# Optimization experiments

Measured on AMD Instinct MI355X. Metric: run time of the kernel, lower is better.

The kernel has to match this reference:

```python
import jax, jax.numpy as jnp
import numpy as np
from jax import lax

B, S, E, H = 4, 1024, 512, 8
D = E // H


def setup_inputs() -> dict:
    key = jax.random.key(0)
    k1, k2, k3 = jax.random.split(key, 3)
    source = jax.random.normal(k1, (B, S, E), dtype=jnp.float32)
    target = jax.random.normal(k2, (B, S, E), dtype=jnp.float32)
    # orthogonal-initialized positional encoder [1, H, 1, D]; random rows are a fine stand-in
    enc = jax.random.normal(k3, (1, H, 1, D), dtype=jnp.float32)
    enc = enc / jnp.linalg.norm(enc, axis=-1, keepdims=True)
    return {
        "source": source,
        "target": target,
        "encoder": enc,
        "alpha": jnp.float32(1.0),
        "beta": jnp.float32(1.0),
        "gamma": jnp.float32(2.0),
    }


def _split_heads(x):
    b, s, e = x.shape
    return x.reshape(b, s, H, e // H).transpose(0, 2, 1, 3)  # [B,H,S,D]


def reference(source, target, encoder, alpha, beta, gamma):
    q = _split_heads(source)  # [B,H,S,D]
    k = _split_heads(target)  # [B,H,S,D]
    pe = encoder[0, :, 0, :]  # [H,D]

    # --- grammar (time) attention: sequential tanh recurrence over t ---
    def step(cc, k_t):
        # cc, k_t: [B,H,D]
        cc = jnp.tanh(cc * pe)
        out = jnp.einsum('bhsd,bhd->bhs', q, cc)  # [B,H,S]
        return k_t * cc, out  # decay_rate = 0.0

    cc0 = k[:, :, 0, :]                      # initial cumulative context
    k_ts = jnp.moveaxis(k, 2, 0)             # [S,B,H,D]
    _, outs = lax.scan(step, cc0, k_ts)      # outs: [S,B,H,S]
    grammar = jnp.moveaxis(outs, 0, 3) / jnp.sqrt(jnp.float32(D))  # [B,H,S,S]
    grammar = jax.nn.softmax(grammar, axis=-1)

    # --- semantic attention ---
    semantic = jnp.einsum('bhsd,bhtd->bhst', q, k) / 100.0  # [B,H,S,S]

    w = jax.nn.softmax((alpha * semantic + beta * grammar) / gamma, axis=-1)

    # merge_heads: [B,H,S,S] -> [B,S,H*S]
    wm = w.transpose(0, 2, 1, 3).reshape(B, S, H * S)
    # output: wm^T @ target -> [B, H*S, E]
    return jnp.matmul(wm.transpose(0, 2, 1), target)
```

## Files before the change

kernel.cpp:

```cpp
#include <hip/hip_runtime.h>
#include <hip/hip_bf16.h>
#include <stdint.h>

#define S_LEN 1024
#define E_DIM 512
#define H_NUM 8
#define D_DIM 64
#define B_NUM 4
#define BH_NUM 32

using s16x8 = __attribute__((ext_vector_type(8))) short;
using f32x4 = __attribute__((ext_vector_type(4))) float;
using us4   = __attribute__((ext_vector_type(4))) unsigned short;

typedef const __attribute__((address_space(1))) uint32_t gas_uint;
typedef __attribute__((address_space(3))) uint32_t las_uint;

static __device__ __forceinline__ unsigned short f2bf(float f) {
  __hip_bfloat16 h = __float2bfloat16(f);
  return __builtin_bit_cast(unsigned short, h);
}
static __device__ __forceinline__ float bf2f(unsigned short u) {
  return __bfloat162float(__builtin_bit_cast(__hip_bfloat16, u));
}

#define NB_RECUR 8
#define NB_PACK  2048
#define NB_TR    512

__global__ __launch_bounds__(256) void k_prep(const float* __restrict__ src,
                                              const float* __restrict__ tgt,
                                              const float* __restrict__ enc,
                                              __hip_bfloat16* __restrict__ qb,
                                              __hip_bfloat16* __restrict__ kb,
                                              __hip_bfloat16* __restrict__ cb,
                                              __hip_bfloat16* __restrict__ tT) {
  __shared__ float tile[64][65];
  const int bid = blockIdx.x;
  const int tid = threadIdx.x;

  if (bid < NB_RECUR) {
    int g = bid * 256 + tid;
    int d = g & 63;
    int bh = g >> 6;
    int h = bh & 7;
    int b = bh >> 3;
    float pe = enc[h * D_DIM + d];
    float pe2 = 2.0f * pe;
    const float* tp = tgt + (size_t)b * S_LEN * E_DIM + h * D_DIM + d;
    __hip_bfloat16* cp = cb + (size_t)bh * S_LEN * D_DIM + d;

    constexpr int CH = 32;
    float bufA[CH], bufB[CH];
#pragma unroll
    for (int i = 0; i < CH; ++i) bufA[i] = tp[(size_t)i * E_DIM];
    float cc = bufA[0];

#pragma unroll 1
    for (int ch = 0; ch < S_LEN / CH; ch += 2) {
      if (ch + 1 < S_LEN / CH) {
#pragma unroll
        for (int i = 0; i < CH; ++i)
          bufB[i] = tp[(size_t)((ch + 1) * CH + i) * E_DIM];
      }
#pragma unroll
      for (int i = 0; i < CH; ++i) {
        float m = cc * pe2;
        float e = __expf(-fabsf(m));
        float th = __builtin_copysignf((1.0f - e) * __builtin_amdgcn_rcpf(1.0f + e), m);
        cp[(size_t)(ch * CH + i) * D_DIM] = __float2bfloat16(th);
        cc = bufA[i] * th;
      }
      if (ch + 2 < S_LEN / CH) {
#pragma unroll
        for (int i = 0; i < CH; ++i)
          bufA[i] = tp[(size_t)((ch + 2) * CH + i) * E_DIM];
      }
#pragma unroll
      for (int i = 0; i < CH; ++i) {
        float m = cc * pe2;
        float e = __expf(-fabsf(m));
        float th = __builtin_copysignf((1.0f - e) * __builtin_amdgcn_rcpf(1.0f + e), m);
        cp[(size_t)((ch + 1) * CH + i) * D_DIM] = __float2bfloat16(th);
        cc = bufB[i] * th;
      }
    }
  } else if (bid < NB_RECUR + NB_PACK) {
    size_t i4 = ((size_t)(bid - NB_RECUR) * 256 + tid) * 4;
    float4 s4 = *reinterpret_cast<const float4*>(src + i4);
    float4 t4 = *reinterpret_cast<const float4*>(tgt + i4);
    int e = (int)(i4 & 511);
    size_t bs = i4 >> 9;
    int s = (int)(bs & 1023);
    int b = (int)(bs >> 10);
    int h = e >> 6, d = e & 63;
    size_t o = (((size_t)(b * H_NUM + h) * S_LEN) + s) * D_DIM + d;
    us4 qv = {f2bf(s4.x), f2bf(s4.y), f2bf(s4.z), f2bf(s4.w)};
    us4 kv = {f2bf(t4.x), f2bf(t4.y), f2bf(t4.z), f2bf(t4.w)};
    *reinterpret_cast<us4*>(qb + o) = qv;
    *reinterpret_cast<us4*>(kb + o) = kv;
  } else {
    int lb = bid - (NB_RECUR + NB_PACK);
    int sx = lb & 15, ey = (lb >> 4) & 7, b = lb >> 7;
    int e0 = ey * 64, s0 = sx * 64;
    int tx = tid & 63, ty = tid >> 6;
    const float* p = tgt + ((size_t)b * S_LEN + s0) * E_DIM + e0;
#pragma unroll
    for (int r = ty; r < 64; r += 4) tile[r][tx] = p[(size_t)r * E_DIM + tx];
    __syncthreads();
    __hip_bfloat16* q = tT + ((size_t)b * E_DIM + e0) * S_LEN + s0;
#pragma unroll
    for (int r = ty; r < 64; r += 4) q[(size_t)r * S_LEN + tx] = __float2bfloat16(tile[tx][r]);
  }
}

__global__ __launch_bounds__(256) void k_weights(const __hip_bfloat16* __restrict__ qb,
                                                 const __hip_bfloat16* __restrict__ kb,
                                                 const __hip_bfloat16* __restrict__ cb,
                                                 __hip_bfloat16* __restrict__ wt,
                                                 const float* __restrict__ pal,
                                                 const float* __restrict__ pbe,
                                                 const float* __restrict__ pga) {
  __shared__ unsigned short stage[4][3][2048];
  __shared__ float red0[4][16];
  __shared__ float red1[4][16];

  const int tid = threadIdx.x;
  const int wave = tid >> 6, lane = tid & 63;
  const int quad = lane >> 4, col = lane & 15;

  const int g = blockIdx.x;
  const int xcd = g & 7;
  const int r = g >> 3;
  const int bh = xcd * 4 + (r >> 6);
  const int s0 = (r & 63) * 16;

  const float alpha = pal[0], beta = pbe[0];
  const float inv_gamma = 1.0f / pga[0];
  const float sa = alpha * 0.01f * inv_gamma;
  const float sb = beta * inv_gamma;

  const __hip_bfloat16* qrow = qb + ((size_t)bh * S_LEN + s0 + col) * D_DIM;
  s16x8 a0 = *reinterpret_cast<const s16x8*>(qrow + quad * 8);
  s16x8 a1 = *reinterpret_cast<const s16x8*>(qrow + 32 + quad * 8);

  const int t_base = wave * 256;
  uint32_t stg[16][2];
  float    stk[16][4];

  const char* cbase = (const char*)(cb + ((size_t)bh * S_LEN + t_base) * D_DIM);
  const char* kbase = (const char*)(kb + ((size_t)bh * S_LEN + t_base) * D_DIM);
  const int so0 = ((lane >> 3) << 7) | (((lane & 7) ^ ((lane >> 3) & 7)) << 4);

  auto stage_it = [&](int it) {
    unsigned short* db = &stage[wave][it % 3][0];
    const char* cs = cbase + it * 2048;
    const char* ks = kbase + it * 2048;
    __builtin_amdgcn_global_load_lds((gas_uint*)(cs + so0),        (las_uint*)(db),        16, 0, 0);
    __builtin_amdgcn_global_load_lds((gas_uint*)(cs + so0 + 1024), (las_uint*)(db + 512),  16, 0, 0);
    __builtin_amdgcn_global_load_lds((gas_uint*)(ks + so0),        (las_uint*)(db + 1024), 16, 0, 0);
    __builtin_amdgcn_global_load_lds((gas_uint*)(ks + so0 + 1024), (las_uint*)(db + 1536), 16, 0, 0);
  };

  stage_it(0);
  stage_it(1);

  const int xswz = (col & 7) << 4;
  float lg[4] = {0.f, 0.f, 0.f, 0.f};
#pragma unroll
  for (int it = 0; it < 16; ++it) {
    if (it < 15) asm volatile("s_waitcnt vmcnt(4)" ::: "memory");
    else         asm volatile("s_waitcnt vmcnt(0)" ::: "memory");
    const char* cw = (const char*)&stage[wave][it % 3][0];
    const char* kw = cw + 2048;
    const int rb = col * 128;
    s16x8 cf0 = *reinterpret_cast<const s16x8*>(cw + rb + ((quad * 16) ^ xswz));
    s16x8 cf1 = *reinterpret_cast<const s16x8*>(cw + rb + ((64 + quad * 16) ^ xswz));
    s16x8 kf0 = *reinterpret_cast<const s16x8*>(kw + rb + ((quad * 16) ^ xswz));
    s16x8 kf1 = *reinterpret_cast<const s16x8*>(kw + rb + ((64 + quad * 16) ^ xswz));
    f32x4 dg = {0.f, 0.f, 0.f, 0.f};
    f32x4 dk = {0.f, 0.f, 0.f, 0.f};
    __builtin_amdgcn_s_setprio(1);
    dg = __builtin_amdgcn_mfma_f32_16x16x32_bf16(a0, cf0, dg, 0, 0, 0);
    dg = __builtin_amdgcn_mfma_f32_16x16x32_bf16(a1, cf1, dg, 0, 0, 0);
    dk = __builtin_amdgcn_mfma_f32_16x16x32_bf16(a0, kf0, dk, 0, 0, 0);
    dk = __builtin_amdgcn_mfma_f32_16x16x32_bf16(a1, kf1, dk, 0, 0, 0);
    __builtin_amdgcn_s_setprio(0);
    if (it + 2 < 16) stage_it(it + 2);
    uint32_t p0 = 0, p1 = 0;
#pragma unroll
    for (int i = 0; i < 4; ++i) {
      float gv = __expf(dg[i] * 0.125f);
      unsigned short u = f2bf(gv);
      lg[i] += bf2f(u);
      if (i < 2) p0 |= (uint32_t)u << (16 * i);
      else       p1 |= (uint32_t)u << (16 * (i - 2));
      stk[it][i] = dk[i];
    }
    stg[it][0] = p0;
    stg[it][1] = p1;
  }
#pragma unroll
  for (int m = 1; m < 16; m <<= 1) {
#pragma unroll
    for (int i = 0; i < 4; ++i) lg[i] += __shfl_xor(lg[i], m);
  }
  if (col == 0) {
#pragma unroll
    for (int i = 0; i < 4; ++i) red0[wave][quad * 4 + i] = lg[i];
  }
  __syncthreads();
  float ilg[4];
#pragma unroll
  for (int i = 0; i < 4; ++i) {
    int rr = quad * 4 + i;
    ilg[i] = 1.0f / (red0[0][rr] + red0[1][rr] + red0[2][rr] + red0[3][rr]);
  }

  float lw[4] = {0.f, 0.f, 0.f, 0.f};
#pragma unroll
  for (int it = 0; it < 16; ++it) {
#pragma unroll
    for (int i = 0; i < 4; ++i) {
      unsigned short u = (unsigned short)((i < 2 ? stg[it][0] >> (16 * i)
                                                 : stg[it][1] >> (16 * (i - 2))) & 0xffffu);
      float gv = bf2f(u) * ilg[i];
      float z = sa * stk[it][i] + sb * gv;
      float wv = __expf(z);
      stk[it][i] = wv;
      lw[i] += wv;
    }
  }
#pragma unroll
  for (int m = 1; m < 16; m <<= 1) {
#pragma unroll
    for (int i = 0; i < 4; ++i) lw[i] += __shfl_xor(lw[i], m);
  }
  if (col == 0) {
#pragma unroll
    for (int i = 0; i < 4; ++i) red1[wave][quad * 4 + i] = lw[i];
  }
  __syncthreads();
  float ilw[4];
#pragma unroll
  for (int i = 0; i < 4; ++i) {
    int rr = quad * 4 + i;
    ilw[i] = 1.0f / (red1[0][rr] + red1[1][rr] + red1[2][rr] + red1[3][rr]);
  }

  __hip_bfloat16* wrow = wt + ((size_t)bh * S_LEN + t_base + col) * S_LEN + s0 + quad * 4;
#pragma unroll
  for (int it = 0; it < 16; ++it) {
    us4 o;
#pragma unroll
    for (int i = 0; i < 4; ++i) o[i] = f2bf(stk[it][i] * ilw[i]);
    *reinterpret_cast<us4*>(wrow + (size_t)it * 16 * S_LEN) = o;
  }
}

__global__ __launch_bounds__(256) void k_outgemm(const __hip_bfloat16* __restrict__ wt,
                                                 const __hip_bfloat16* __restrict__ tT,
                                                 float* __restrict__ out) {
  __shared__ __hip_bfloat16 As[2][128 * 64];
  __shared__ __hip_bfloat16 Bs[2][128 * 64];
  const int tid = threadIdx.x;
  const int wave = tid >> 6, lane = tid & 63;
  const int quad = lane >> 4, col = lane & 15;

  const int g = blockIdx.x;
  const int xcd = g & 7;
  const int local = g >> 3;
  const int strip = xcd * 32 + (local >> 2);
  const int ntile = local & 3;
  const int bh = strip >> 3;
  const int mt = strip & 7;
  const int b = bh >> 3;
  const int m0 = mt * 128;
  const int n0 = ntile * 128;

  const __hip_bfloat16* Ag = wt + (size_t)bh * S_LEN * S_LEN;
  const __hip_bfloat16* Bg = tT + (size_t)b * E_DIM * S_LEN;
  const int mw = (wave >> 1) * 64, nw = (wave & 1) * 64;
  const int lrow = lane >> 3;
  const int lcolswz = ((lane & 7) ^ lrow) * 8;

  f32x4 acc[4][4];
#pragma unroll
  for (int i = 0; i < 4; ++i)
#pragma unroll
    for (int j = 0; j < 4; ++j) acc[i][j] = (f32x4){0.f, 0.f, 0.f, 0.f};

  auto stage = [&](int kt, int buf) {
    const int k0 = kt * 64;
#pragma unroll
    for (int j = 0; j < 4; ++j) {
      const int rbase = j * 32 + wave * 8;
      const __hip_bfloat16* gpA = Ag + (size_t)(m0 + rbase + lrow) * S_LEN + k0 + lcolswz;
      __builtin_amdgcn_global_load_lds((gas_uint*)gpA,
                                       (las_uint*)(&As[buf][rbase * 64]), 16, 0, 0);
      const __hip_bfloat16* gpB = Bg + (size_t)(n0 + rbase + lrow) * S_LEN + k0 + lcolswz;
      __builtin_amdgcn_global_load_lds((gas_uint*)gpB,
                                       (las_uint*)(&Bs[buf][rbase * 64]), 16, 0, 0);
    }
  };

  const int swz = (col & 7) << 4;
  auto compute = [&](int buf) {
    const char* Ab = (const char*)&As[buf][0];
    const char* Bb = (const char*)&Bs[buf][0];
    __builtin_amdgcn_s_setprio(1);
#pragma unroll
    for (int ks = 0; ks < 2; ++ks) {
      s16x8 af[4], bfr[4];
#pragma unroll
      for (int i = 0; i < 4; ++i)
        af[i] = *reinterpret_cast<const s16x8*>(
            Ab + (size_t)(mw + i * 16 + col) * 128 + ((ks * 64 + quad * 16) ^ swz));
#pragma unroll
      for (int i = 0; i < 4; ++i)
        bfr[i] = *reinterpret_cast<const s16x8*>(
            Bb + (size_t)(nw + i * 16 + col) * 128 + ((ks * 64 + quad * 16) ^ swz));
#pragma unroll
      for (int mi = 0; mi < 4; ++mi)
#pragma unroll
        for (int ni = 0; ni < 4; ++ni)
          acc[mi][ni] = __builtin_amdgcn_mfma_f32_16x16x32_bf16(af[mi], bfr[ni], acc[mi][ni], 0, 0, 0);
    }
    __builtin_amdgcn_s_setprio(0);
  };

  stage(0, 0);
#pragma unroll 1
  for (int kt = 0; kt < 15; ++kt) {
    stage(kt + 1, (kt + 1) & 1);
    asm volatile("s_waitcnt vmcnt(8)" ::: "memory");
    __builtin_amdgcn_s_barrier();
    compute(kt & 1);
    asm volatile("" ::: "memory");
    __builtin_amdgcn_s_barrier();
  }
  asm volatile("s_waitcnt vmcnt(0)" ::: "memory");
  __builtin_amdgcn_s_barrier();
  compute(1);

#pragma unroll
  for (int mi = 0; mi < 4; ++mi)
#pragma unroll
    for (int ni = 0; ni < 4; ++ni)
#pragma unroll
      for (int i = 0; i < 4; ++i) {
        int m = m0 + mw + mi * 16 + quad * 4 + i;
        int n = n0 + nw + ni * 16 + col;
        out[((size_t)bh * S_LEN + m) * E_DIM + n] = acc[mi][ni][i];
      }
}

extern "C" void kernel_launch(void* const* d_in, const int* in_sizes, int n_in,
                              void* d_out, int out_size, void* d_ws, size_t ws_size,
                              hipStream_t stream) {
  (void)in_sizes; (void)n_in; (void)out_size; (void)ws_size;
  const float* src = (const float*)d_in[0];
  const float* tgt = (const float*)d_in[1];
  const float* enc = (const float*)d_in[2];
  const float* pal = (const float*)d_in[3];
  const float* pbe = (const float*)d_in[4];
  const float* pga = (const float*)d_in[5];
  float* out = (float*)d_out;

  char* ws = (char*)d_ws;
  __hip_bfloat16* qb = (__hip_bfloat16*)(ws);
  __hip_bfloat16* kb = (__hip_bfloat16*)(ws + ((size_t)4 << 20));
  __hip_bfloat16* cb = (__hip_bfloat16*)(ws + ((size_t)8 << 20));
  __hip_bfloat16* tT = (__hip_bfloat16*)(ws + ((size_t)12 << 20));
  __hip_bfloat16* wt = (__hip_bfloat16*)(ws + ((size_t)16 << 20));

  k_prep<<<NB_RECUR + NB_PACK + NB_TR, 256, 0, stream>>>(src, tgt, enc, qb, kb, cb, tT);
  k_weights<<<dim3((S_LEN / 16) * BH_NUM), 256, 0, stream>>>(qb, kb, cb, wt, pal, pbe, pga);
  k_outgemm<<<dim3((E_DIM / 128) * (S_LEN / 128) * BH_NUM), 256, 0, stream>>>(wt, tT, out);
}
```

Baseline: 204.3 us.

## Process 32 query rows per block with 8 waves in weights kernel

The weights kernel now handles 32 query rows per block instead of 16, using 512 threads (8 waves) that each cover 128 key positions. Every staged C/K tile fragment feeds two MFMA row groups, so global and LDS traffic for the cumulative-context and key tiles per query row is halved. In exchange, per-thread register state for the staged values stays about the same, LDS use doubles to 8 staging buffers, and the grid has half as many blocks.

New measurement: 207.4 us. Within noise of the previous version (+1.5%).

```diff
diff --git a/kernel.cpp b/kernel.cpp
--- a/kernel.cpp
+++ b/kernel.cpp
@@ -114,16 +114,16 @@
   }
 }
 
-__global__ __launch_bounds__(256) void k_weights(const __hip_bfloat16* __restrict__ qb,
+__global__ __launch_bounds__(512) void k_weights(const __hip_bfloat16* __restrict__ qb,
                                                  const __hip_bfloat16* __restrict__ kb,
                                                  const __hip_bfloat16* __restrict__ cb,
                                                  __hip_bfloat16* __restrict__ wt,
                                                  const float* __restrict__ pal,
                                                  const float* __restrict__ pbe,
                                                  const float* __restrict__ pga) {
-  __shared__ unsigned short stage[4][3][2048];
-  __shared__ float red0[4][16];
-  __shared__ float red1[4][16];
+  __shared__ unsigned short stage[8][3][2048];
+  __shared__ float red0[8][32];
+  __shared__ float red1[8][32];
 
   const int tid = threadIdx.x;
   const int wave = tid >> 6, lane = tid & 63;
@@ -132,8 +132,8 @@
   const int g = blockIdx.x;
   const int xcd = g & 7;
   const int r = g >> 3;
-  const int bh = xcd * 4 + (r >> 6);
-  const int s0 = (r & 63) * 16;
+  const int bh = xcd * 4 + (r >> 5);
+  const int s0 = (r & 31) * 32;
 
   const float alpha = pal[0], beta = pbe[0];
   const float inv_gamma = 1.0f / pga[0];
@@ -143,10 +143,12 @@
   const __hip_bfloat16* qrow = qb + ((size_t)bh * S_LEN + s0 + col) * D_DIM;
   s16x8 a0 = *reinterpret_cast<const s16x8*>(qrow + quad * 8);
   s16x8 a1 = *reinterpret_cast<const s16x8*>(qrow + 32 + quad * 8);
-
-  const int t_base = wave * 256;
-  uint32_t stg[16][2];
-  float    stk[16][4];
+  s16x8 a2 = *reinterpret_cast<const s16x8*>(qrow + 16 * D_DIM + quad * 8);
+  s16x8 a3 = *reinterpret_cast<const s16x8*>(qrow + 16 * D_DIM + 32 + quad * 8);
+
+  const int t_base = wave * 128;
+  uint32_t stg0[8][2], stg1[8][2];
+  float    stk0[8][4], stk1[8][4];
 
   const char* cbase = (const char*)(cb + ((size_t)bh * S_LEN + t_base) * D_DIM);
   const char* kbase = (const char*)(kb + ((size_t)bh * S_LEN + t_base) * D_DIM);
@@ -166,11 +168,12 @@
   stage_it(1);
 
   const int xswz = (col & 7) << 4;
-  float lg[4] = {0.f, 0.f, 0.f, 0.f};
-#pragma unroll
-  for (int it = 0; it < 16; ++it) {
-    if (it < 15) asm volatile("s_waitcnt vmcnt(4)" ::: "memory");
-    else         asm volatile("s_waitcnt vmcnt(0)" ::: "memory");
+  float lg0[4] = {0.f, 0.f, 0.f, 0.f};
+  float lg1[4] = {0.f, 0.f, 0.f, 0.f};
+#pragma unroll
+  for (int it = 0; it < 8; ++it) {
+    if (it < 7) asm volatile("s_waitcnt vmcnt(4)" ::: "memory");
+    else        asm volatile("s_waitcnt vmcnt(0)" ::: "memory");
     const char* cw = (const char*)&stage[wave][it % 3][0];
     const char* kw = cw + 2048;
     const int rb = col * 128;
@@ -178,83 +181,125 @@
     s16x8 cf1 = *reinterpret_cast<const s16x8*>(cw + rb + ((64 + quad * 16) ^ xswz));
     s16x8 kf0 = *reinterpret_cast<const s16x8*>(kw + rb + ((quad * 16) ^ xswz));
     s16x8 kf1 = *reinterpret_cast<const s16x8*>(kw + rb + ((64 + quad * 16) ^ xswz));
-    f32x4 dg = {0.f, 0.f, 0.f, 0.f};
-    f32x4 dk = {0.f, 0.f, 0.f, 0.f};
+    f32x4 dg0 = {0.f, 0.f, 0.f, 0.f};
+    f32x4 dg1 = {0.f, 0.f, 0.f, 0.f};
+    f32x4 dk0 = {0.f, 0.f, 0.f, 0.f};
+    f32x4 dk1 = {0.f, 0.f, 0.f, 0.f};
     __builtin_amdgcn_s_setprio(1);
-    dg = __builtin_amdgcn_mfma_f32_16x16x32_bf16(a0, cf0, dg, 0, 0, 0);
-    dg = __builtin_amdgcn_mfma_f32_16x16x32_bf16(a1, cf1, dg, 0, 0, 0);
-    dk = __builtin_amdgcn_mfma_f32_16x16x32_bf16(a0, kf0, dk, 0, 0, 0);
-    dk = __builtin_amdgcn_mfma_f32_16x16x32_bf16(a1, kf1, dk, 0, 0, 0);
+    dg0 = __builtin_amdgcn_mfma_f32_16x16x32_bf16(a0, cf0, dg0, 0, 0, 0);
+    dg0 = __builtin_amdgcn_mfma_f32_16x16x32_bf16(a1, cf1, dg0, 0, 0, 0);
+    dg1 = __builtin_amdgcn_mfma_f32_16x16x32_bf16(a2, cf0, dg1, 0, 0, 0);
+    dg1 = __builtin_amdgcn_mfma_f32_16x16x32_bf16(a3, cf1, dg1, 0, 0, 0);
+    dk0 = __builtin_amdgcn_mfma_f32_16x16x32_bf16(a0, kf0, dk0, 0, 0, 0);
+    dk0 = __builtin_amdgcn_mfma_f32_16x16x32_bf16(a1, kf1, dk0, 0, 0, 0);
+    dk1 = __builtin_amdgcn_mfma_f32_16x16x32_bf16(a2, kf0, dk1, 0, 0, 0);
+    dk1 = __builtin_amdgcn_mfma_f32_16x16x32_bf16(a3, kf1, dk1, 0, 0, 0);
     __builtin_amdgcn_s_setprio(0);
-    if (it + 2 < 16) stage_it(it + 2);
-    uint32_t p0 = 0, p1 = 0;
-#pragma unroll
-    for (int i = 0; i < 4; ++i) {
-      float gv = __expf(dg[i] * 0.125f);
-      unsigned short u = f2bf(gv);
-      lg[i] += bf2f(u);
-      if (i < 2) p0 |= (uint32_t)u << (16 * i);
-      else       p1 |= (uint32_t)u << (16 * (i - 2));
-      stk[it][i] = dk[i];
-    }
-    stg[it][0] = p0;
-    stg[it][1] = p1;
+    if (it + 2 < 8) stage_it(it + 2);
+    uint32_t p0 = 0, p1 = 0, q0 = 0, q1 = 0;
+#pragma unroll
+    for (int i = 0; i < 4; ++i) {
+      float gv0 = __expf(dg0[i] * 0.125f);
+      float gv1 = __expf(dg1[i] * 0.125f);
+      unsigned short u0 = f2bf(gv0);
+      unsigned short u1 = f2bf(gv1);
+      lg0[i] += bf2f(u0);
+      lg1[i] += bf2f(u1);
+      if (i < 2) { p0 |= (uint32_t)u0 << (16 * i);       q0 |= (uint32_t)u1 << (16 * i); }
+      else       { p1 |= (uint32_t)u0 << (16 * (i - 2)); q1 |= (uint32_t)u1 << (16 * (i - 2)); }
+      stk0[it][i] = dk0[i];
+      stk1[it][i] = dk1[i];
+    }
+    stg0[it][0] = p0; stg0[it][1] = p1;
+    stg1[it][0] = q0; stg1[it][1] = q1;
   }
 #pragma unroll
   for (int m = 1; m < 16; m <<= 1) {
 #pragma unroll
-    for (int i = 0; i < 4; ++i) lg[i] += __shfl_xor(lg[i], m);
+    for (int i = 0; i < 4; ++i) {
+      lg0[i] += __shfl_xor(lg0[i], m);
+      lg1[i] += __shfl_xor(lg1[i], m);
+    }
   }
   if (col == 0) {
 #pragma unroll
-    for (int i = 0; i < 4; ++i) red0[wave][quad * 4 + i] = lg[i];
+    for (int i = 0; i < 4; ++i) {
+      red0[wave][quad * 4 + i]      = lg0[i];
+      red0[wave][16 + quad * 4 + i] = lg1[i];
+    }
   }
   __syncthreads();
-  float ilg[4];
+  float ilg0[4], ilg1[4];
 #pragma unroll
   for (int i = 0; i < 4; ++i) {
-    int rr = quad * 4 + i;
-    ilg[i] = 1.0f / (red0[0][rr] + red0[1][rr] + red0[2][rr] + red0[3][rr]);
-  }
-
-  float lw[4] = {0.f, 0.f, 0.f, 0.f};
-#pragma unroll
-  for (int it = 0; it < 16; ++it) {
-#pragma unroll
-    for (int i = 0; i < 4; ++i) {
-      unsigned short u = (unsigned short)((i < 2 ? stg[it][0] >> (16 * i)
-                                                 : stg[it][1] >> (16 * (i - 2))) & 0xffffu);
-      float gv = bf2f(u) * ilg[i];
-      float z = sa * stk[it][i] + sb * gv;
-      float wv = __expf(z);
-      stk[it][i] = wv;
-      lw[i] += wv;
+    int r0 = quad * 4 + i, r1 = 16 + quad * 4 + i;
+    float s0a = 0.f, s1a = 0.f;
+#pragma unroll
+    for (int w = 0; w < 8; ++w) { s0a += red0[w][r0]; s1a += red0[w][r1]; }
+    ilg0[i] = 1.0f / s0a;
+    ilg1[i] = 1.0f / s1a;
+  }
+
+  float lw0[4] = {0.f, 0.f, 0.f, 0.f};
+  float lw1[4] = {0.f, 0.f, 0.f, 0.f};
+#pragma unroll
+  for (int it = 0; it < 8; ++it) {
+#pragma unroll
+    for (int i = 0; i < 4; ++i) {
+      unsigned short u0 = (unsigned short)((i < 2 ? stg0[it][0] >> (16 * i)
+                                                  : stg0[it][1] >> (16 * (i - 2))) & 0xffffu);
+      unsigned short u1 = (unsigned short)((i < 2 ? stg1[it][0] >> (16 * i)
+                                                  : stg1[it][1] >> (16 * (i - 2))) & 0xffffu);
+      float gv0 = bf2f(u0) * ilg0[i];
+      float gv1 = bf2f(u1) * ilg1[i];
+      float z0 = sa * stk0[it][i] + sb * gv0;
+      float z1 = sa * stk1[it][i] + sb * gv1;
+      float wv0 = __expf(z0);
+      float wv1 = __expf(z1);
+      stk0[it][i] = wv0;
+      stk1[it][i] = wv1;
+      lw0[i] += wv0;
+      lw1[i] += wv1;
     }
   }
 #pragma unroll
   for (int m = 1; m < 16; m <<= 1) {
 #pragma unroll
-    for (int i = 0; i < 4; ++i) lw[i] += __shfl_xor(lw[i], m);
+    for (int i = 0; i < 4; ++i) {
+      lw0[i] += __shfl_xor(lw0[i], m);
+      lw1[i] += __shfl_xor(lw1[i], m);
+    }
   }
   if (col == 0) {
 #pragma unroll
-    for (int i = 0; i < 4; ++i) red1[wave][quad * 4 + i] = lw[i];
+    for (int i = 0; i < 4; ++i) {
+      red1[wave][quad * 4 + i]      = lw0[i];
+      red1[wave][16 + quad * 4 + i] = lw1[i];
+    }
   }
   __syncthreads();
-  float ilw[4];
+  float ilw0[4], ilw1[4];
 #pragma unroll
   for (int i = 0; i < 4; ++i) {
-    int rr = quad * 4 + i;
-    ilw[i] = 1.0f / (red1[0][rr] + red1[1][rr] + red1[2][rr] + red1[3][rr]);
+    int r0 = quad * 4 + i, r1 = 16 + quad * 4 + i;
+    float s0a = 0.f, s1a = 0.f;
+#pragma unroll
+    for (int w = 0; w < 8; ++w) { s0a += red1[w][r0]; s1a += red1[w][r1]; }
+    ilw0[i] = 1.0f / s0a;
+    ilw1[i] = 1.0f / s1a;
   }
 
   __hip_bfloat16* wrow = wt + ((size_t)bh * S_LEN + t_base + col) * S_LEN + s0 + quad * 4;
 #pragma unroll
-  for (int it = 0; it < 16; ++it) {
-    us4 o;
-#pragma unroll
-    for (int i = 0; i < 4; ++i) o[i] = f2bf(stk[it][i] * ilw[i]);
-    *reinterpret_cast<us4*>(wrow + (size_t)it * 16 * S_LEN) = o;
+  for (int it = 0; it < 8; ++it) {
+    us4 o0, o1;
+#pragma unroll
+    for (int i = 0; i < 4; ++i) {
+      o0[i] = f2bf(stk0[it][i] * ilw0[i]);
+      o1[i] = f2bf(stk1[it][i] * ilw1[i]);
+    }
+    *reinterpret_cast<us4*>(wrow + (size_t)it * 16 * S_LEN)      = o0;
+    *reinterpret_cast<us4*>(wrow + (size_t)it * 16 * S_LEN + 16) = o1;
   }
 }
 
@@ -375,6 +420,6 @@
   __hip_bfloat16* wt = (__hip_bfloat16*)(ws + ((size_t)16 << 20));
 
   k_prep<<<NB_RECUR + NB_PACK + NB_TR, 256, 0, stream>>>(src, tgt, enc, qb, kb, cb, tT);
-  k_weights<<<dim3((S_LEN / 16) * BH_NUM), 256, 0, stream>>>(qb, kb, cb, wt, pal, pbe, pga);
+  k_weights<<<dim3((S_LEN / 32) * BH_NUM), 512, 0, stream>>>(qb, kb, cb, wt, pal, pbe, pga);
   k_outgemm<<<dim3((E_DIM / 128) * (S_LEN / 128) * BH_NUM), 256, 0, stream>>>(wt, tT, out);
 }
```
